# Performance work log

Measured on AMD Instinct MI355X. Metric: run time of the kernel, lower is better.

The kernel has to match this reference:

```python
import jax, jax.numpy as jnp
import numpy as np

EPS_KERNEL = 1e-6
EPS_Z = 1e-6


def softmax_kernel(data, projection_matrix):
    # data: [b,h,l,d], projection_matrix: [m,d]
    data_normalizer = data.shape[-1] ** (-0.25)
    data = data * data_normalizer
    projection = jnp.einsum('bhld,md->bhlm', data, projection_matrix)
    data_squared_norm = jnp.sum(data ** 2, axis=-1, keepdims=True) / 2
    return jnp.exp(projection - data_squared_norm + EPS_KERNEL)


def setup_inputs() -> dict:
    key = jax.random.key(0)
    k1, k2, k3, k4 = jax.random.split(key, 4)
    b, h, l, d, m = 4, 8, 8192, 64, 256
    return {
        'q': jax.random.normal(k1, (b, h, l, d), dtype=jnp.float32),
        'k': jax.random.normal(k2, (b, h, l, d), dtype=jnp.float32),
        'v': jax.random.normal(k3, (b, h, l, d), dtype=jnp.float32),
        'projection_matrix': jax.random.normal(k4, (m, d), dtype=jnp.float32),
    }


def reference(q, k, v, projection_matrix):
    q_prime = softmax_kernel(q, projection_matrix)  # [b,h,l,m]
    k_prime = softmax_kernel(k, projection_matrix)  # [b,h,l,m]
    kv = jnp.einsum('bhlm,bhld->bhmd', k_prime, v)  # [b,h,m,d]
    k_sum = jnp.sum(k_prime, axis=2)                # [b,h,m]
    z_raw = jnp.einsum('bhlm,bhm->bhl', q_prime, k_sum)
    z = 1.0 / (z_raw + EPS_Z)                       # [b,h,l]
    # (q_prime @ kv) scaled per-token by z
    out = jnp.einsum('bhlm,bhmd->bhld', q_prime, kv) * z[..., None]
    return out
```

## Files before the change

kernel.cpp:

```cpp
#include <hip/hip_runtime.h>
#include <hip/hip_bf16.h>


#define BH 32
#define LL 8192
#define DD 64
#define MM 256
#define NRM 0.35355339059327373f
#define SQS 0.0625f
#define EPSK 1e-6f
#define EPSZ 1e-6f

typedef __attribute__((ext_vector_type(8))) short bf16x8;
typedef __attribute__((ext_vector_type(4))) float f32x4;
#define MFMA(a, b, c) __builtin_amdgcn_mfma_f32_16x16x32_bf16(a, b, c, 0, 0, 0)

static __device__ __forceinline__ short f2bf(float x) {
    union { float f; unsigned u; } c{x};
    unsigned r = c.u + 0x7fffu + ((c.u >> 16) & 1u);
    return (short)(r >> 16);
}

static __device__ __forceinline__ void load_pfrags(
    const float* __restrict__ Pm, int wv, int quad, int l16, bf16x8 pb[2][4])
{
#pragma unroll
    for (int ks = 0; ks < 2; ++ks)
#pragma unroll
        for (int mt = 0; mt < 4; ++mt) {
            const float* pr = Pm + (wv * 64 + mt * 16 + l16) * DD + ks * 32 + quad * 8;
            float4 p0 = *(const float4*)pr;
            float4 p1 = *(const float4*)(pr + 4);
            bf16x8 f;
            f[0] = f2bf(p0.x * NRM); f[1] = f2bf(p0.y * NRM);
            f[2] = f2bf(p0.z * NRM); f[3] = f2bf(p0.w * NRM);
            f[4] = f2bf(p1.x * NRM); f[5] = f2bf(p1.y * NRM);
            f[6] = f2bf(p1.z * NRM); f[7] = f2bf(p1.w * NRM);
            pb[ks][mt] = f;
        }
}

__global__ __launch_bounds__(256, 2) void kv_kernel(
    const float* __restrict__ kin, const float* __restrict__ vin,
    const float* __restrict__ Pm, float* __restrict__ kv, float* __restrict__ ksum)
{
    __shared__ short Kb[32 * 72];
    __shared__ short Vt[64 * 40];
    __shared__ short Ktp[256 * 40];
    __shared__ float cl_lds[32];

    const int t = threadIdx.x;
    const int lane = t & 63, wv = t >> 6;
    const int quad = lane >> 4, l16 = lane & 15;
    const int bh = blockIdx.x >> 4, chunk = blockIdx.x & 15;

    bf16x8 pb[2][4];
    load_pfrags(Pm, wv, quad, l16, pb);

    f32x4 kvacc[4][4];
#pragma unroll
    for (int mt = 0; mt < 4; ++mt)
#pragma unroll
        for (int dt = 0; dt < 4; ++dt) kvacc[mt][dt] = (f32x4)0.f;
    float ksacc[4] = {0.f, 0.f, 0.f, 0.f};

    const size_t base = ((size_t)bh * LL + (size_t)chunk * 512) * DD;
    const float* kb = kin + base;
    const float* vb = vin + base;
    const int sl = t >> 4, sd4 = t & 15;

    for (int tile = 0; tile < 16; ++tile) {
        __syncthreads();
#pragma unroll
        for (int half = 0; half < 2; ++half) {
            const int l = sl + half * 16;
            const int gi = (tile * 32 + l) * DD + sd4 * 4;
            float4 kf = *(const float4*)(kb + gi);
            float sq = kf.x * kf.x + kf.y * kf.y + kf.z * kf.z + kf.w * kf.w;
            sq += __shfl_xor(sq, 1); sq += __shfl_xor(sq, 2);
            sq += __shfl_xor(sq, 4); sq += __shfl_xor(sq, 8);
            if (sd4 == 0) cl_lds[l] = EPSK - SQS * sq;
            union { short s[4]; unsigned long long u; } uk;
            uk.s[0] = f2bf(kf.x); uk.s[1] = f2bf(kf.y);
            uk.s[2] = f2bf(kf.z); uk.s[3] = f2bf(kf.w);
            *(unsigned long long*)&Kb[l * 72 + sd4 * 4] = uk.u;
            float4 vf = *(const float4*)(vb + gi);
            Vt[(sd4 * 4 + 0) * 40 + l] = f2bf(vf.x);
            Vt[(sd4 * 4 + 1) * 40 + l] = f2bf(vf.y);
            Vt[(sd4 * 4 + 2) * 40 + l] = f2bf(vf.z);
            Vt[(sd4 * 4 + 3) * 40 + l] = f2bf(vf.w);
        }
        __syncthreads();
        f32x4 pt[2][4];
#pragma unroll
        for (int lt = 0; lt < 2; ++lt)
#pragma unroll
            for (int mt = 0; mt < 4; ++mt) pt[lt][mt] = (f32x4)0.f;
#pragma unroll
        for (int ks = 0; ks < 2; ++ks)
#pragma unroll
            for (int lt = 0; lt < 2; ++lt) {
                bf16x8 af = *(bf16x8*)&Kb[(lt * 16 + l16) * 72 + ks * 32 + quad * 8];
#pragma unroll
                for (int mt = 0; mt < 4; ++mt)
                    pt[lt][mt] = MFMA(af, pb[ks][mt], pt[lt][mt]);
            }
        float cl[2][4];
#pragma unroll
        for (int lt = 0; lt < 2; ++lt)
#pragma unroll
            for (int r = 0; r < 4; ++r) cl[lt][r] = cl_lds[lt * 16 + quad * 4 + r];
#pragma unroll
        for (int lt = 0; lt < 2; ++lt)
#pragma unroll
            for (int mt = 0; mt < 4; ++mt) {
                union { short s[4]; unsigned long long u; } uo;
#pragma unroll
                for (int r = 0; r < 4; ++r) {
                    float w = __expf(pt[lt][mt][r] + cl[lt][r]);
                    ksacc[mt] += w;
                    uo.s[r] = f2bf(w);
                }
                *(unsigned long long*)&Ktp[(wv * 64 + mt * 16 + l16) * 40 + lt * 16 + quad * 4] = uo.u;
            }
        bf16x8 aK[4], bV[4];
#pragma unroll
        for (int mt = 0; mt < 4; ++mt)
            aK[mt] = *(bf16x8*)&Ktp[(wv * 64 + mt * 16 + l16) * 40 + quad * 8];
#pragma unroll
        for (int dt = 0; dt < 4; ++dt)
            bV[dt] = *(bf16x8*)&Vt[(dt * 16 + l16) * 40 + quad * 8];
#pragma unroll
        for (int mt = 0; mt < 4; ++mt)
#pragma unroll
            for (int dt = 0; dt < 4; ++dt)
                kvacc[mt][dt] = MFMA(aK[mt], bV[dt], kvacc[mt][dt]);
    }
    float* kvg = kv + (size_t)bh * MM * DD;
#pragma unroll
    for (int mt = 0; mt < 4; ++mt) {
        float r = ksacc[mt];
        r += __shfl_xor(r, 16); r += __shfl_xor(r, 32);
        if (quad == 0) atomicAdd(ksum + bh * MM + wv * 64 + mt * 16 + l16, r);
#pragma unroll
        for (int dt = 0; dt < 4; ++dt)
#pragma unroll
            for (int rg = 0; rg < 4; ++rg)
                atomicAdd(kvg + (wv * 64 + mt * 16 + quad * 4 + rg) * DD + dt * 16 + l16,
                          kvacc[mt][dt][rg]);
    }
}

__global__ __launch_bounds__(256, 2) void out_kernel(
    const float* __restrict__ qin, const float* __restrict__ Pm,
    const float* __restrict__ kv, const float* __restrict__ ksum,
    float* __restrict__ out)
{
    __shared__ short Qb[32 * 72];
    __shared__ short Qp[32 * 264];
    __shared__ short kvT[64 * 264];
    __shared__ float ks_lds[MM];
    __shared__ float cl_lds[32];
    __shared__ float z_lds[32];

    const int t = threadIdx.x;
    const int lane = t & 63, wv = t >> 6;
    const int quad = lane >> 4, l16 = lane & 15;
    const int bh = blockIdx.x >> 4, chunk = blockIdx.x & 15;

    bf16x8 pb[2][4];
    load_pfrags(Pm, wv, quad, l16, pb);

    const float* kvg = kv + (size_t)bh * MM * DD;
#pragma unroll
    for (int it = 0; it < 16; ++it) {
        int i = t + it * 256;
        int m = i >> 4, d4 = i & 15;
        float4 f = *(const float4*)(kvg + m * DD + d4 * 4);
        kvT[(d4 * 4 + 0) * 264 + m] = f2bf(f.x);
        kvT[(d4 * 4 + 1) * 264 + m] = f2bf(f.y);
        kvT[(d4 * 4 + 2) * 264 + m] = f2bf(f.z);
        kvT[(d4 * 4 + 3) * 264 + m] = f2bf(f.w);
    }
    ks_lds[t] = ksum[bh * MM + t];
    __syncthreads();
    float ksv[4];
#pragma unroll
    for (int mt = 0; mt < 4; ++mt) ksv[mt] = ks_lds[wv * 64 + mt * 16 + l16];

    const size_t base = ((size_t)bh * LL + (size_t)chunk * 512) * DD;
    const float* qb = qin + base;
    float* ob = out + base;
    const int sl = t >> 4, sd4 = t & 15;

    for (int tile = 0; tile < 16; ++tile) {
        __syncthreads();
        if (t < 32) z_lds[t] = 0.f;
#pragma unroll
        for (int half = 0; half < 2; ++half) {
            const int l = sl + half * 16;
            const int gi = (tile * 32 + l) * DD + sd4 * 4;
            float4 qf = *(const float4*)(qb + gi);
            float sq = qf.x * qf.x + qf.y * qf.y + qf.z * qf.z + qf.w * qf.w;
            sq += __shfl_xor(sq, 1); sq += __shfl_xor(sq, 2);
            sq += __shfl_xor(sq, 4); sq += __shfl_xor(sq, 8);
            if (sd4 == 0) cl_lds[l] = EPSK - SQS * sq;
            union { short s[4]; unsigned long long u; } uq;
            uq.s[0] = f2bf(qf.x); uq.s[1] = f2bf(qf.y);
            uq.s[2] = f2bf(qf.z); uq.s[3] = f2bf(qf.w);
            *(unsigned long long*)&Qb[l * 72 + sd4 * 4] = uq.u;
        }
        __syncthreads();
        f32x4 pt[2][4];
#pragma unroll
        for (int lt = 0; lt < 2; ++lt)
#pragma unroll
            for (int mt = 0; mt < 4; ++mt) pt[lt][mt] = (f32x4)0.f;
#pragma unroll
        for (int ks = 0; ks < 2; ++ks)
#pragma unroll
            for (int lt = 0; lt < 2; ++lt) {
                bf16x8 af = *(bf16x8*)&Qb[(lt * 16 + l16) * 72 + ks * 32 + quad * 8];
#pragma unroll
                for (int mt = 0; mt < 4; ++mt)
                    pt[lt][mt] = MFMA(af, pb[ks][mt], pt[lt][mt]);
            }
        float cl[2][4];
#pragma unroll
        for (int lt = 0; lt < 2; ++lt)
#pragma unroll
            for (int r = 0; r < 4; ++r) cl[lt][r] = cl_lds[lt * 16 + quad * 4 + r];
        float zp[2][4] = {{0.f,0.f,0.f,0.f},{0.f,0.f,0.f,0.f}};
#pragma unroll
        for (int lt = 0; lt < 2; ++lt)
#pragma unroll
            for (int mt = 0; mt < 4; ++mt)
#pragma unroll
                for (int r = 0; r < 4; ++r) {
                    float w = __expf(pt[lt][mt][r] + cl[lt][r]);
                    zp[lt][r] += w * ksv[mt];
                    Qp[(lt * 16 + quad * 4 + r) * 264 + wv * 64 + mt * 16 + l16] = f2bf(w);
                }
#pragma unroll
        for (int lt = 0; lt < 2; ++lt)
#pragma unroll
            for (int r = 0; r < 4; ++r) {
                float vz = zp[lt][r];
                vz += __shfl_xor(vz, 1); vz += __shfl_xor(vz, 2);
                vz += __shfl_xor(vz, 4); vz += __shfl_xor(vz, 8);
                if (l16 == 0) atomicAdd(&z_lds[lt * 16 + quad * 4 + r], vz);
            }
        __syncthreads();
        f32x4 oc[2];
        oc[0] = (f32x4)0.f; oc[1] = (f32x4)0.f;
#pragma unroll
        for (int ks = 0; ks < 8; ++ks) {
            bf16x8 bk = *(bf16x8*)&kvT[(wv * 16 + l16) * 264 + ks * 32 + quad * 8];
#pragma unroll
            for (int lt = 0; lt < 2; ++lt) {
                bf16x8 aq = *(bf16x8*)&Qp[(lt * 16 + l16) * 264 + ks * 32 + quad * 8];
                oc[lt] = MFMA(aq, bk, oc[lt]);
            }
        }
#pragma unroll
        for (int lt = 0; lt < 2; ++lt)
#pragma unroll
            for (int r = 0; r < 4; ++r) {
                const int row = lt * 16 + quad * 4 + r;
                const float z = 1.f / (z_lds[row] + EPSZ);
                ob[(size_t)(tile * 32 + row) * DD + wv * 16 + l16] = oc[lt][r] * z;
            }
    }
}

extern "C" void kernel_launch(void* const* d_in, const int* in_sizes, int n_in,
                              void* d_out, int out_size, void* d_ws, size_t ws_size,
                              hipStream_t stream) {
    const float* q  = (const float*)d_in[0];
    const float* k  = (const float*)d_in[1];
    const float* v  = (const float*)d_in[2];
    const float* Pm = (const float*)d_in[3];

    float* kvw = (float*)d_ws;
    float* ksw = kvw + (size_t)BH * MM * DD;

    hipMemsetAsync(d_ws, 0, ((size_t)BH * MM * DD + (size_t)BH * MM) * sizeof(float), stream);
    hipLaunchKernelGGL(kv_kernel, dim3(512), dim3(256), 0, stream, k, v, Pm, kvw, ksw);
    hipLaunchKernelGGL(out_kernel, dim3(512), dim3(256), 0, stream, q, Pm, kvw, ksw, (float*)d_out);
}
```

Before: 324.5 us.

## Prefetch tiles into registers, double grid, alias LDS, and remap block order

The grid doubles to 1024 blocks of 256 rows each, and blocks are remapped so consecutive block ids spread across different bh. Each tile's global loads are software-prefetched into registers one tile ahead. In out_kernel, the kvT and Qp LDS buffers share one region, with kv fragments hoisted into registers, and the projection MFMA is transposed so the z reduction needs fewer shuffles. Launch bounds are raised for higher occupancy. The costs are more kv/ksum atomics per bh and higher register pressure, which could spill under the tighter launch bounds.

```diff
diff --git a/kernel.cpp b/kernel.cpp
--- a/kernel.cpp
+++ b/kernel.cpp
@@ -10,6 +10,8 @@
 #define SQS 0.0625f
 #define EPSK 1e-6f
 #define EPSZ 1e-6f
+#define NTILE 8
+#define RPB 256
 
 typedef __attribute__((ext_vector_type(8))) short bf16x8;
 typedef __attribute__((ext_vector_type(4))) float f32x4;
@@ -19,6 +21,11 @@
     union { float f; unsigned u; } c{x};
     unsigned r = c.u + 0x7fffu + ((c.u >> 16) & 1u);
     return (short)(r >> 16);
+}
+
+static __device__ __forceinline__ void decode_block(int i, int& bh, int& chunk) {
+    bh = ((i & 7) << 2) | ((i >> 3) & 3);
+    chunk = i >> 5;
 }
 
 static __device__ __forceinline__ void load_pfrags(
@@ -40,7 +47,7 @@
         }
 }
 
-__global__ __launch_bounds__(256, 2) void kv_kernel(
+__global__ __launch_bounds__(256, 3) void kv_kernel(
     const float* __restrict__ kin, const float* __restrict__ vin,
     const float* __restrict__ Pm, float* __restrict__ kv, float* __restrict__ ksum)
 {
@@ -52,7 +59,8 @@
     const int t = threadIdx.x;
     const int lane = t & 63, wv = t >> 6;
     const int quad = lane >> 4, l16 = lane & 15;
-    const int bh = blockIdx.x >> 4, chunk = blockIdx.x & 15;
+    int bh, chunk;
+    decode_block(blockIdx.x, bh, chunk);
 
     bf16x8 pb[2][4];
     load_pfrags(Pm, wv, quad, l16, pb);
@@ -64,18 +72,26 @@
         for (int dt = 0; dt < 4; ++dt) kvacc[mt][dt] = (f32x4)0.f;
     float ksacc[4] = {0.f, 0.f, 0.f, 0.f};
 
-    const size_t base = ((size_t)bh * LL + (size_t)chunk * 512) * DD;
+    const size_t base = ((size_t)bh * LL + (size_t)chunk * RPB) * DD;
     const float* kb = kin + base;
     const float* vb = vin + base;
     const int sl = t >> 4, sd4 = t & 15;
 
-    for (int tile = 0; tile < 16; ++tile) {
+    float4 kreg[2], vreg[2];
+#pragma unroll
+    for (int half = 0; half < 2; ++half) {
+        const int gi = (sl + half * 16) * DD + sd4 * 4;
+        kreg[half] = *(const float4*)(kb + gi);
+        vreg[half] = *(const float4*)(vb + gi);
+    }
+
+    for (int tile = 0; tile < NTILE; ++tile) {
         __syncthreads();
 #pragma unroll
         for (int half = 0; half < 2; ++half) {
             const int l = sl + half * 16;
-            const int gi = (tile * 32 + l) * DD + sd4 * 4;
-            float4 kf = *(const float4*)(kb + gi);
+            const float4 kf = kreg[half];
+            const float4 vf = vreg[half];
             float sq = kf.x * kf.x + kf.y * kf.y + kf.z * kf.z + kf.w * kf.w;
             sq += __shfl_xor(sq, 1); sq += __shfl_xor(sq, 2);
             sq += __shfl_xor(sq, 4); sq += __shfl_xor(sq, 8);
@@ -84,52 +100,51 @@
             uk.s[0] = f2bf(kf.x); uk.s[1] = f2bf(kf.y);
             uk.s[2] = f2bf(kf.z); uk.s[3] = f2bf(kf.w);
             *(unsigned long long*)&Kb[l * 72 + sd4 * 4] = uk.u;
-            float4 vf = *(const float4*)(vb + gi);
             Vt[(sd4 * 4 + 0) * 40 + l] = f2bf(vf.x);
             Vt[(sd4 * 4 + 1) * 40 + l] = f2bf(vf.y);
             Vt[(sd4 * 4 + 2) * 40 + l] = f2bf(vf.z);
             Vt[(sd4 * 4 + 3) * 40 + l] = f2bf(vf.w);
         }
-        __syncthreads();
-        f32x4 pt[2][4];
-#pragma unroll
-        for (int lt = 0; lt < 2; ++lt)
-#pragma unroll
-            for (int mt = 0; mt < 4; ++mt) pt[lt][mt] = (f32x4)0.f;
-#pragma unroll
-        for (int ks = 0; ks < 2; ++ks)
-#pragma unroll
-            for (int lt = 0; lt < 2; ++lt) {
-                bf16x8 af = *(bf16x8*)&Kb[(lt * 16 + l16) * 72 + ks * 32 + quad * 8];
+        if (tile + 1 < NTILE) {
+#pragma unroll
+            for (int half = 0; half < 2; ++half) {
+                const int gi = ((tile + 1) * 32 + sl + half * 16) * DD + sd4 * 4;
+                kreg[half] = *(const float4*)(kb + gi);
+                vreg[half] = *(const float4*)(vb + gi);
+            }
+        }
+        __syncthreads();
+#pragma unroll
+        for (int lt = 0; lt < 2; ++lt) {
+            f32x4 ptl[4];
+#pragma unroll
+            for (int mt = 0; mt < 4; ++mt) ptl[mt] = (f32x4)0.f;
+#pragma unroll
+            for (int ks = 0; ks < 2; ++ks) {
+                const bf16x8 af = *(const bf16x8*)&Kb[(lt * 16 + l16) * 72 + ks * 32 + quad * 8];
 #pragma unroll
                 for (int mt = 0; mt < 4; ++mt)
-                    pt[lt][mt] = MFMA(af, pb[ks][mt], pt[lt][mt]);
-            }
-        float cl[2][4];
-#pragma unroll
-        for (int lt = 0; lt < 2; ++lt)
-#pragma unroll
-            for (int r = 0; r < 4; ++r) cl[lt][r] = cl_lds[lt * 16 + quad * 4 + r];
-#pragma unroll
-        for (int lt = 0; lt < 2; ++lt)
+                    ptl[mt] = MFMA(af, pb[ks][mt], ptl[mt]);
+            }
 #pragma unroll
             for (int mt = 0; mt < 4; ++mt) {
                 union { short s[4]; unsigned long long u; } uo;
 #pragma unroll
                 for (int r = 0; r < 4; ++r) {
-                    float w = __expf(pt[lt][mt][r] + cl[lt][r]);
+                    const float w = __expf(ptl[mt][r] + cl_lds[lt * 16 + quad * 4 + r]);
                     ksacc[mt] += w;
                     uo.s[r] = f2bf(w);
                 }
                 *(unsigned long long*)&Ktp[(wv * 64 + mt * 16 + l16) * 40 + lt * 16 + quad * 4] = uo.u;
             }
+        }
         bf16x8 aK[4], bV[4];
 #pragma unroll
         for (int mt = 0; mt < 4; ++mt)
-            aK[mt] = *(bf16x8*)&Ktp[(wv * 64 + mt * 16 + l16) * 40 + quad * 8];
+            aK[mt] = *(const bf16x8*)&Ktp[(wv * 64 + mt * 16 + l16) * 40 + quad * 8];
 #pragma unroll
         for (int dt = 0; dt < 4; ++dt)
-            bV[dt] = *(bf16x8*)&Vt[(dt * 16 + l16) * 40 + quad * 8];
+            bV[dt] = *(const bf16x8*)&Vt[(dt * 16 + l16) * 40 + quad * 8];
 #pragma unroll
         for (int mt = 0; mt < 4; ++mt)
 #pragma unroll
@@ -151,14 +166,13 @@
     }
 }
 
-__global__ __launch_bounds__(256, 2) void out_kernel(
+__global__ __launch_bounds__(256, 4) void out_kernel(
     const float* __restrict__ qin, const float* __restrict__ Pm,
     const float* __restrict__ kv, const float* __restrict__ ksum,
     float* __restrict__ out)
 {
+    __shared__ short sm[64 * 264];
     __shared__ short Qb[32 * 72];
-    __shared__ short Qp[32 * 264];
-    __shared__ short kvT[64 * 264];
     __shared__ float ks_lds[MM];
     __shared__ float cl_lds[32];
     __shared__ float z_lds[32];
@@ -166,7 +180,8 @@
     const int t = threadIdx.x;
     const int lane = t & 63, wv = t >> 6;
     const int quad = lane >> 4, l16 = lane & 15;
-    const int bh = blockIdx.x >> 4, chunk = blockIdx.x & 15;
+    int bh, chunk;
+    decode_block(blockIdx.x, bh, chunk);
 
     bf16x8 pb[2][4];
     load_pfrags(Pm, wv, quad, l16, pb);
@@ -174,33 +189,39 @@
     const float* kvg = kv + (size_t)bh * MM * DD;
 #pragma unroll
     for (int it = 0; it < 16; ++it) {
-        int i = t + it * 256;
-        int m = i >> 4, d4 = i & 15;
-        float4 f = *(const float4*)(kvg + m * DD + d4 * 4);
-        kvT[(d4 * 4 + 0) * 264 + m] = f2bf(f.x);
-        kvT[(d4 * 4 + 1) * 264 + m] = f2bf(f.y);
-        kvT[(d4 * 4 + 2) * 264 + m] = f2bf(f.z);
-        kvT[(d4 * 4 + 3) * 264 + m] = f2bf(f.w);
+        const int i = t + it * 256;
+        const int m = i >> 4, d4 = i & 15;
+        const float4 f = *(const float4*)(kvg + m * DD + d4 * 4);
+        sm[(d4 * 4 + 0) * 264 + m] = f2bf(f.x);
+        sm[(d4 * 4 + 1) * 264 + m] = f2bf(f.y);
+        sm[(d4 * 4 + 2) * 264 + m] = f2bf(f.z);
+        sm[(d4 * 4 + 3) * 264 + m] = f2bf(f.w);
     }
     ks_lds[t] = ksum[bh * MM + t];
     __syncthreads();
-    float ksv[4];
-#pragma unroll
-    for (int mt = 0; mt < 4; ++mt) ksv[mt] = ks_lds[wv * 64 + mt * 16 + l16];
-
-    const size_t base = ((size_t)bh * LL + (size_t)chunk * 512) * DD;
+
+    bf16x8 bk[8];
+#pragma unroll
+    for (int ks = 0; ks < 8; ++ks)
+        bk[ks] = *(const bf16x8*)&sm[(wv * 16 + l16) * 264 + ks * 32 + quad * 8];
+
+    const size_t base = ((size_t)bh * LL + (size_t)chunk * RPB) * DD;
     const float* qb = qin + base;
     float* ob = out + base;
     const int sl = t >> 4, sd4 = t & 15;
 
-    for (int tile = 0; tile < 16; ++tile) {
+    float4 qreg[2];
+#pragma unroll
+    for (int half = 0; half < 2; ++half)
+        qreg[half] = *(const float4*)(qb + (sl + half * 16) * DD + sd4 * 4);
+
+    for (int tile = 0; tile < NTILE; ++tile) {
         __syncthreads();
         if (t < 32) z_lds[t] = 0.f;
 #pragma unroll
         for (int half = 0; half < 2; ++half) {
             const int l = sl + half * 16;
-            const int gi = (tile * 32 + l) * DD + sd4 * 4;
-            float4 qf = *(const float4*)(qb + gi);
+            const float4 qf = qreg[half];
             float sq = qf.x * qf.x + qf.y * qf.y + qf.z * qf.z + qf.w * qf.w;
             sq += __shfl_xor(sq, 1); sq += __shfl_xor(sq, 2);
             sq += __shfl_xor(sq, 4); sq += __shfl_xor(sq, 8);
@@ -210,66 +231,70 @@
             uq.s[2] = f2bf(qf.z); uq.s[3] = f2bf(qf.w);
             *(unsigned long long*)&Qb[l * 72 + sd4 * 4] = uq.u;
         }
-        __syncthreads();
-        f32x4 pt[2][4];
-#pragma unroll
-        for (int lt = 0; lt < 2; ++lt)
-#pragma unroll
-            for (int mt = 0; mt < 4; ++mt) pt[lt][mt] = (f32x4)0.f;
-#pragma unroll
-        for (int ks = 0; ks < 2; ++ks)
-#pragma unroll
-            for (int lt = 0; lt < 2; ++lt) {
-                bf16x8 af = *(bf16x8*)&Qb[(lt * 16 + l16) * 72 + ks * 32 + quad * 8];
-#pragma unroll
-                for (int mt = 0; mt < 4; ++mt)
-                    pt[lt][mt] = MFMA(af, pb[ks][mt], pt[lt][mt]);
-            }
-        float cl[2][4];
-#pragma unroll
-        for (int lt = 0; lt < 2; ++lt)
-#pragma unroll
-            for (int r = 0; r < 4; ++r) cl[lt][r] = cl_lds[lt * 16 + quad * 4 + r];
-        float zp[2][4] = {{0.f,0.f,0.f,0.f},{0.f,0.f,0.f,0.f}};
-#pragma unroll
-        for (int lt = 0; lt < 2; ++lt)
-#pragma unroll
-            for (int mt = 0; mt < 4; ++mt)
-#pragma unroll
-                for (int r = 0; r < 4; ++r) {
-                    float w = __expf(pt[lt][mt][r] + cl[lt][r]);
-                    zp[lt][r] += w * ksv[mt];
-                    Qp[(lt * 16 + quad * 4 + r) * 264 + wv * 64 + mt * 16 + l16] = f2bf(w);
-                }
-#pragma unroll
-        for (int lt = 0; lt < 2; ++lt)
+        if (tile + 1 < NTILE) {
+#pragma unroll
+            for (int half = 0; half < 2; ++half)
+                qreg[half] = *(const float4*)(qb + ((tile + 1) * 32 + sl + half * 16) * DD + sd4 * 4);
+        }
+        __syncthreads();
+
+        bf16x8 qf2[2][2];
+#pragma unroll
+        for (int ks2 = 0; ks2 < 2; ++ks2)
+#pragma unroll
+            for (int lt = 0; lt < 2; ++lt)
+                qf2[ks2][lt] = *(const bf16x8*)&Qb[(lt * 16 + l16) * 72 + ks2 * 32 + quad * 8];
+        const float clv0 = cl_lds[l16];
+        const float clv1 = cl_lds[16 + l16];
+        float zp0 = 0.f, zp1 = 0.f;
+#pragma unroll
+        for (int mt = 0; mt < 4; ++mt) {
+            f32x4 pt0 = (f32x4)0.f, pt1 = (f32x4)0.f;
+#pragma unroll
+            for (int ks2 = 0; ks2 < 2; ++ks2) {
+                pt0 = MFMA(pb[ks2][mt], qf2[ks2][0], pt0);
+                pt1 = MFMA(pb[ks2][mt], qf2[ks2][1], pt1);
+            }
+            const float4 km4 = *(const float4*)&ks_lds[wv * 64 + mt * 16 + quad * 4];
+            const float km[4] = {km4.x, km4.y, km4.z, km4.w};
+            union { short s[4]; unsigned long long u; } u0, u1;
 #pragma unroll
             for (int r = 0; r < 4; ++r) {
-                float vz = zp[lt][r];
-                vz += __shfl_xor(vz, 1); vz += __shfl_xor(vz, 2);
-                vz += __shfl_xor(vz, 4); vz += __shfl_xor(vz, 8);
-                if (l16 == 0) atomicAdd(&z_lds[lt * 16 + quad * 4 + r], vz);
-            }
-        __syncthreads();
-        f32x4 oc[2];
-        oc[0] = (f32x4)0.f; oc[1] = (f32x4)0.f;
+                const float w0 = __expf(pt0[r] + clv0);
+                const float w1 = __expf(pt1[r] + clv1);
+                zp0 += w0 * km[r];
+                zp1 += w1 * km[r];
+                u0.s[r] = f2bf(w0);
+                u1.s[r] = f2bf(w1);
+            }
+            *(unsigned long long*)&sm[(l16) * 264 + wv * 64 + mt * 16 + quad * 4] = u0.u;
+            *(unsigned long long*)&sm[(16 + l16) * 264 + wv * 64 + mt * 16 + quad * 4] = u1.u;
+        }
+        zp0 += __shfl_xor(zp0, 16); zp0 += __shfl_xor(zp0, 32);
+        zp1 += __shfl_xor(zp1, 16); zp1 += __shfl_xor(zp1, 32);
+        if (lane < 16) {
+            atomicAdd(&z_lds[l16], zp0);
+            atomicAdd(&z_lds[16 + l16], zp1);
+        }
+        __syncthreads();
+
+        f32x4 oc0 = (f32x4)0.f, oc1 = (f32x4)0.f;
 #pragma unroll
         for (int ks = 0; ks < 8; ++ks) {
-            bf16x8 bk = *(bf16x8*)&kvT[(wv * 16 + l16) * 264 + ks * 32 + quad * 8];
-#pragma unroll
-            for (int lt = 0; lt < 2; ++lt) {
-                bf16x8 aq = *(bf16x8*)&Qp[(lt * 16 + l16) * 264 + ks * 32 + quad * 8];
-                oc[lt] = MFMA(aq, bk, oc[lt]);
-            }
-        }
-#pragma unroll
-        for (int lt = 0; lt < 2; ++lt)
-#pragma unroll
-            for (int r = 0; r < 4; ++r) {
-                const int row = lt * 16 + quad * 4 + r;
-                const float z = 1.f / (z_lds[row] + EPSZ);
-                ob[(size_t)(tile * 32 + row) * DD + wv * 16 + l16] = oc[lt][r] * z;
-            }
+            const bf16x8 aq0 = *(const bf16x8*)&sm[(l16) * 264 + ks * 32 + quad * 8];
+            const bf16x8 aq1 = *(const bf16x8*)&sm[(16 + l16) * 264 + ks * 32 + quad * 8];
+            oc0 = MFMA(aq0, bk[ks], oc0);
+            oc1 = MFMA(aq1, bk[ks], oc1);
+        }
+#pragma unroll
+        for (int r = 0; r < 4; ++r) {
+            const int row0 = quad * 4 + r;
+            const float z0 = 1.f / (z_lds[row0] + EPSZ);
+            ob[(size_t)(tile * 32 + row0) * DD + wv * 16 + l16] = oc0[r] * z0;
+            const int row1 = 16 + quad * 4 + r;
+            const float z1 = 1.f / (z_lds[row1] + EPSZ);
+            ob[(size_t)(tile * 32 + row1) * DD + wv * 16 + l16] = oc1[r] * z1;
+        }
     }
 }
 
@@ -285,6 +310,6 @@
     float* ksw = kvw + (size_t)BH * MM * DD;
 
     hipMemsetAsync(d_ws, 0, ((size_t)BH * MM * DD + (size_t)BH * MM) * sizeof(float), stream);
-    hipLaunchKernelGGL(kv_kernel, dim3(512), dim3(256), 0, stream, k, v, Pm, kvw, ksw);
-    hipLaunchKernelGGL(out_kernel, dim3(512), dim3(256), 0, stream, q, Pm, kvw, ksw, (float*)d_out);
-}
+    hipLaunchKernelGGL(kv_kernel, dim3(1024), dim3(256), 0, stream, k, v, Pm, kvw, ksw);
+    hipLaunchKernelGGL(out_kernel, dim3(1024), dim3(256), 0, stream, q, Pm, kvw, ksw, (float*)d_out);
+}
```

Result: slower. 399.5 us (+23.1%).
